# Optimization experiments

Hardware: AMD Instinct MI355X
Metric: run time of the kernel (lower is better)

The kernel has to match this reference:

```python
import jax, jax.numpy as jnp
import numpy as np

N_NODES = 100000
N_EDGES = 1600000
OBS_DIMS = 128
HID = 128
ACT_DIMS = 8
NUM_GRAPHS = 256
NEG_SLOPE = 0.2


def setup_inputs() -> dict:
    key = jax.random.key(0)
    ks = jax.random.split(key, 20)
    inp = {}
    inp["x"] = jax.random.normal(ks[0], (N_NODES, OBS_DIMS), dtype=jnp.float32)
    inp["edge_index"] = jax.random.randint(ks[1], (2, N_EDGES), 0, N_NODES, dtype=jnp.int64)
    inp["batch"] = jnp.sort(jax.random.randint(ks[2], (N_NODES,), 0, NUM_GRAPHS, dtype=jnp.int64))
    # GATConv layer params (heads=1): W [out,in], att_src/att_dst [out], bias [out]
    dims = [(HID, OBS_DIMS), (HID, HID), (HID, HID)]
    for i, (o, c) in enumerate(dims, start=1):
        k = 3 + 4 * (i - 1)
        inp[f"W{i}"] = jax.random.normal(ks[k], (o, c), dtype=jnp.float32) * (1.0 / np.sqrt(c))
        inp[f"as{i}"] = jax.random.normal(ks[k + 1], (o,), dtype=jnp.float32) * 0.1
        inp[f"ad{i}"] = jax.random.normal(ks[k + 2], (o,), dtype=jnp.float32) * 0.1
        inp[f"b{i}"] = jnp.zeros((o,), dtype=jnp.float32)
    inp["Wl"] = jax.random.normal(ks[15], (ACT_DIMS, HID), dtype=jnp.float32) * (1.0 / np.sqrt(HID))
    inp["bl"] = jnp.zeros((ACT_DIMS,), dtype=jnp.float32)
    return inp


def _gat_conv(x, src, dst, W, att_src, att_dst, bias):
    """PyG GATConv with heads=1, negative_slope=0.2 (self-loops already in src/dst)."""
    h = x @ W.T                                  # [N, out]
    a_s = h @ att_src                            # [N]
    a_d = h @ att_dst                            # [N]
    e = jax.nn.leaky_relu(a_s[src] + a_d[dst], NEG_SLOPE)   # [E] per-edge logits
    m = jax.ops.segment_max(e, dst, num_segments=N_NODES)   # segment softmax (stable)
    ex = jnp.exp(e - m[dst])
    denom = jax.ops.segment_sum(ex, dst, num_segments=N_NODES)
    alpha = ex / denom[dst]                      # [E]
    out = jax.ops.segment_sum(alpha[:, None] * h[src], dst, num_segments=N_NODES)
    return out + bias


def reference(x, edge_index, batch, W1, as1, ad1, b1, W2, as2, ad2, b2,
              W3, as3, ad3, b3, Wl, bl):
    # add self-loops (PyG GATConv default add_self_loops=True)
    loop = jnp.arange(N_NODES, dtype=edge_index.dtype)
    src = jnp.concatenate([edge_index[0], loop])
    dst = jnp.concatenate([edge_index[1], loop])

    h = jax.nn.relu(_gat_conv(x, src, dst, W1, as1, ad1, b1))
    h = jax.nn.relu(_gat_conv(h, src, dst, W2, as2, ad2, b2))
    h = jax.nn.relu(_gat_conv(h, src, dst, W3, as3, ad3, b3))
    h = jnp.tanh(h @ Wl.T + bl)                  # [N, act_dims]

    # global_mean_pool over graph ids
    sums = jax.ops.segment_sum(h, batch, num_segments=NUM_GRAPHS)
    cnts = jax.ops.segment_sum(jnp.ones((h.shape[0],), h.dtype), batch, num_segments=NUM_GRAPHS)
    return sums / jnp.clip(cnts, 1.0)[:, None]
```

## Files before the change

kernel.cpp:

```cpp
#include <hip/hip_runtime.h>

#define N_NODES 100000
#define N_EDGES 1600000
#define E_TOT   1700000
#define HID     128
#define NGRAPH  256
#define NBUCK   196
#define NBLK1   831
#define HSTRIDE 832

typedef unsigned short ushort_t;
typedef unsigned int uint_t;
typedef __attribute__((ext_vector_type(8))) short bf16x8;
typedef __attribute__((ext_vector_type(4))) float f32x4;

__device__ inline ushort_t f2bf(float f) {
  uint_t u = __float_as_uint(f);
  return (ushort_t)((u + 0x7FFFu + ((u >> 16) & 1u)) >> 16);
}

__global__ __launch_bounds__(256) void k_wcvt(const float* __restrict__ W0,
                                              const float* __restrict__ W1,
                                              const float* __restrict__ W2,
                                              const float* __restrict__ Wlh,
                                              ushort_t* __restrict__ Wb,
                                              ushort_t* __restrict__ Wlb) {
  int i = blockIdx.x * 256 + threadIdx.x;
  if (i < 49152) {
    const float* src = (i < 16384) ? W0 : (i < 32768 ? W1 : W2);
    Wb[i] = f2bf(src[i & 16383]);
  } else if (i < 51200) {
    int j = i - 49152;
    Wlb[j] = (j < 1024) ? f2bf(Wlh[j]) : (ushort_t)0;
  }
}

__global__ __launch_bounds__(256) void k_b1(const int* __restrict__ ei,
                                            int* __restrict__ hist) {
  __shared__ int h[NBUCK];
  const int t = threadIdx.x;
  for (int i = t; i < NBUCK; i += 256) h[i] = 0;
  __syncthreads();
  const int e0 = blockIdx.x * 2048;
#pragma unroll
  for (int u = 0; u < 8; ++u) {
    int e = e0 + u * 256 + t;
    if (e < E_TOT) {
      int dst = (e < N_EDGES) ? ei[N_EDGES + e] : (e - N_EDGES);
      atomicAdd(&h[dst >> 9], 1);
    }
  }
  __syncthreads();
  for (int i = t; i < NBUCK; i += 256) hist[i * HSTRIDE + blockIdx.x] = h[i];
}

__global__ __launch_bounds__(1024) void k_bscan1(int* __restrict__ hist,
                                                 int* __restrict__ btot) {
  __shared__ int sh[1024];
  const int b = blockIdx.x, t = threadIdx.x;
  int v = (t < NBLK1) ? hist[b * HSTRIDE + t] : 0;
  sh[t] = v;
  __syncthreads();
  for (int off = 1; off < 1024; off <<= 1) {
    int x = (t >= off) ? sh[t - off] : 0;
    __syncthreads();
    sh[t] += x;
    __syncthreads();
  }
  if (t < NBLK1) hist[b * HSTRIDE + t] = sh[t] - v;
  if (t == 1023) btot[b] = sh[1023];
}

__global__ void k_bscan2(const int* __restrict__ btot, int* __restrict__ bbase) {
  if (threadIdx.x == 0 && blockIdx.x == 0) {
    int run = 0;
    for (int i = 0; i < NBUCK; ++i) { bbase[i] = run; run += btot[i]; }
    bbase[NBUCK] = run;
  }
}

__global__ __launch_bounds__(256) void k_b2(const int* __restrict__ ei,
                                            const int* __restrict__ hist,
                                            const int* __restrict__ bbase,
                                            int2* __restrict__ buf) {
  __shared__ int h[NBUCK];
  __shared__ int base2[NBUCK];
  const int t = threadIdx.x;
  for (int i = t; i < NBUCK; i += 256) {
    h[i] = 0;
    base2[i] = bbase[i] + hist[i * HSTRIDE + blockIdx.x];
  }
  __syncthreads();
  const int e0 = blockIdx.x * 2048;
#pragma unroll
  for (int u = 0; u < 8; ++u) {
    int e = e0 + u * 256 + t;
    if (e < E_TOT) {
      int src, dst;
      if (e < N_EDGES) { src = ei[e]; dst = ei[N_EDGES + e]; }
      else             { src = e - N_EDGES; dst = src; }
      int bk = dst >> 9;
      int r = atomicAdd(&h[bk], 1);
      buf[base2[bk] + r] = int2{src, dst};
    }
  }
}

__global__ __launch_bounds__(512) void k_b3(const int2* __restrict__ buf,
                                            const int* __restrict__ bbase,
                                            int* __restrict__ indptr,
                                            int* __restrict__ csr_src) {
  __shared__ int cnt[512];
  __shared__ int cur[512];
  const int b = blockIdx.x, t = threadIdx.x;
  cnt[t] = 0;
  __syncthreads();
  const int es = bbase[b], ee = bbase[b + 1];
  for (int e = es + t; e < ee; e += 512) {
    int2 p = buf[e];
    atomicAdd(&cnt[p.y & 511], 1);
  }
  __syncthreads();
  int v = cnt[t];
  cur[t] = v;
  __syncthreads();
  for (int off = 1; off < 512; off <<= 1) {
    int x = (t >= off) ? cur[t - off] : 0;
    __syncthreads();
    cur[t] += x;
    __syncthreads();
  }
  int excl = cur[t] - v;
  int n = b * 512 + t;
  if (n < N_NODES) indptr[n] = es + excl;
  if (b == NBUCK - 1 && t == 0) indptr[N_NODES] = E_TOT;
  __syncthreads();
  cur[t] = es + excl;
  __syncthreads();
  for (int e = es + t; e < ee; e += 512) {
    int2 p = buf[e];
    int pos = atomicAdd(&cur[p.y & 511], 1);
    csr_src[pos] = p.x;
  }
}

template <bool IN_F32>
__global__ __launch_bounds__(256) void k_gemm(const void* __restrict__ Xin,
                                              const ushort_t* __restrict__ Wbl,
                                              const float* __restrict__ att_s,
                                              const float* __restrict__ att_d,
                                              ushort_t* __restrict__ Hb,
                                              float* __restrict__ As,
                                              float* __restrict__ Ad) {
  __shared__ ushort_t Wl[128 * 128];
  __shared__ ushort_t Xl[64 * 128];
  const int t = threadIdx.x;
  const int row0 = blockIdx.x * 64;

#pragma unroll
  for (int i = 0; i < 8; ++i) {
    int idx = (t + i * 256) << 3;
    int o = idx >> 7, c = idx & 127;
    uint4 wv = *(const uint4*)&Wbl[idx];
    *(uint4*)((char*)Wl + o * 256 + ((c * 2) ^ ((o & 7) << 4))) = wv;
  }
  if (IN_F32) {
    const float* X = (const float*)Xin;
#pragma unroll
    for (int i = 0; i < 8; ++i) {
      int idx = (t + i * 256) << 2;
      int r = idx >> 7, c = idx & 127;
      int row = row0 + r;
      float4 xv = (row < N_NODES) ? *(const float4*)&X[row * 128 + c]
                                  : float4{0.f, 0.f, 0.f, 0.f};
      ushort4 xb{f2bf(xv.x), f2bf(xv.y), f2bf(xv.z), f2bf(xv.w)};
      *(ushort4*)((char*)Xl + r * 256 + ((c * 2) ^ ((r & 7) << 4))) = xb;
    }
  } else {
    const ushort_t* X = (const ushort_t*)Xin;
#pragma unroll
    for (int i = 0; i < 4; ++i) {
      int idx = (t + i * 256) << 3;
      int r = idx >> 7, c = idx & 127;
      int row = row0 + r;
      uint4 xv = (row < N_NODES) ? *(const uint4*)&X[row * 128 + c]
                                 : uint4{0u, 0u, 0u, 0u};
      *(uint4*)((char*)Xl + r * 256 + ((c * 2) ^ ((r & 7) << 4))) = xv;
    }
  }
  __syncthreads();

  const int wv = t >> 6;
  const int lane = t & 63;
  const int lr = lane & 15;
  const int lg = lane >> 4;
  f32x4 acc[8] = {};

#pragma unroll
  for (int ks = 0; ks < 4; ++ks) {
    const int kbyte = ks * 64 + lg * 16;
    const int arow = wv * 16 + lr;
    bf16x8 afrag = *(const bf16x8*)((char*)Xl + arow * 256 +
                                    (kbyte ^ ((arow & 7) << 4)));
#pragma unroll
    for (int ot = 0; ot < 8; ++ot) {
      const int orow = ot * 16 + lr;
      bf16x8 bfrag = *(const bf16x8*)((char*)Wl + orow * 256 +
                                      (kbyte ^ ((orow & 7) << 4)));
      acc[ot] = __builtin_amdgcn_mfma_f32_16x16x32_bf16(afrag, bfrag, acc[ot],
                                                        0, 0, 0);
    }
  }

  float ps[4] = {0.f, 0.f, 0.f, 0.f}, pd[4] = {0.f, 0.f, 0.f, 0.f};
#pragma unroll
  for (int ot = 0; ot < 8; ++ot) {
    float sa = att_s[ot * 16 + lr], sd = att_d[ot * 16 + lr];
#pragma unroll
    for (int j = 0; j < 4; ++j) {
      ps[j] += acc[ot][j] * sa;
      pd[j] += acc[ot][j] * sd;
    }
  }
#pragma unroll
  for (int m = 1; m < 16; m <<= 1) {
#pragma unroll
    for (int j = 0; j < 4; ++j) {
      ps[j] += __shfl_xor(ps[j], m);
      pd[j] += __shfl_xor(pd[j], m);
    }
  }
  if (lr == 0) {
#pragma unroll
    for (int j = 0; j < 4; ++j) {
      int row = row0 + wv * 16 + lg * 4 + j;
      if (row < N_NODES) { As[row] = ps[j]; Ad[row] = pd[j]; }
    }
  }

  __syncthreads();
#pragma unroll
  for (int ot = 0; ot < 8; ++ot)
#pragma unroll
    for (int j = 0; j < 4; ++j) {
      int r = wv * 16 + lg * 4 + j;
      int cbyte = (ot * 16 + lr) * 2;
      *(ushort_t*)((char*)Xl + r * 256 + (cbyte ^ ((r & 7) << 4))) =
          f2bf(acc[ot][j]);
    }
  __syncthreads();
#pragma unroll
  for (int i = 0; i < 4; ++i) {
    int idx = t + i * 256;
    int r = idx >> 4, u = idx & 15;
    int row = row0 + r;
    if (row < N_NODES)
      *(uint4*)&Hb[row * 128 + u * 8] =
          *(const uint4*)((char*)Xl + r * 256 + ((u * 16) ^ ((r & 7) << 4)));
  }
}

__global__ __launch_bounds__(256) void k_agg(const ushort_t* __restrict__ Hb,
                                             const float* __restrict__ a_s,
                                             const float* __restrict__ a_d,
                                             const int* __restrict__ indptr,
                                             const int* __restrict__ csr_src,
                                             const float* __restrict__ bias,
                                             ushort_t* __restrict__ OUTb) {
  const int lane = threadIdx.x & 63;
  const int wid  = threadIdx.x >> 6;
  const int half = lane >> 5;
  const int l32  = lane & 31;
  const int n = blockIdx.x * 8 + wid * 2 + half;

  const int start = indptr[n];
  const int deg   = indptr[n + 1] - start;
  const float adn = a_d[n];

  int   s0 = csr_src[start + ((l32 < deg) ? l32 : 0)];
  float w0 = 0.f;
  if (l32 < deg) {
    float e = a_s[s0] + adn;
    e = (e > 0.f) ? e : 0.2f * e;
    w0 = __expf(e);
  }
  float wsum = w0;

  const int degA = __shfl(deg, 0);
  const int degB = __shfl(deg, 32);
  const int degM = max(degA, degB);

  const int q  = lane >> 4;
  const int qe = q & 1;
  const int srcbase = (q >> 1) << 5;
  const int ch = (lane & 15) << 3;
  float acc8[8] = {0.f, 0.f, 0.f, 0.f, 0.f, 0.f, 0.f, 0.f};

#define FMA8(W4, A)                                                         \
  {                                                                         \
    float a_ = (A);                                                         \
    acc8[0] += a_ * __uint_as_float((W4).x << 16);                          \
    acc8[1] += a_ * __uint_as_float((W4).x & 0xFFFF0000u);                  \
    acc8[2] += a_ * __uint_as_float((W4).y << 16);                          \
    acc8[3] += a_ * __uint_as_float((W4).y & 0xFFFF0000u);                  \
    acc8[4] += a_ * __uint_as_float((W4).z << 16);                          \
    acc8[5] += a_ * __uint_as_float((W4).z & 0xFFFF0000u);                  \
    acc8[6] += a_ * __uint_as_float((W4).w << 16);                          \
    acc8[7] += a_ * __uint_as_float((W4).w & 0xFFFF0000u);                  \
  }

  {
    const int npM = (min(degM, 32) + 1) >> 1;
    float av[8]; int sv[8];
#pragma unroll
    for (int u = 0; u < 8; ++u) {
      int sl = srcbase + ((u << 1) + qe);
      av[u] = __shfl(w0, sl);
      sv[u] = __shfl(s0, sl);
    }
    uint4 hvA[4], hvB[4];
#pragma unroll
    for (int u = 0; u < 4; ++u)
      if (u < npM) hvA[u] = *(const uint4*)&Hb[sv[u] * 128 + ch];
#pragma unroll
    for (int u = 0; u < 4; ++u)
      if (u + 4 < npM) hvB[u] = *(const uint4*)&Hb[sv[u + 4] * 128 + ch];
#pragma unroll
    for (int u = 0; u < 4; ++u)
      if (u < npM) FMA8(hvA[u], av[u]);
#pragma unroll
    for (int u = 0; u < 4; ++u)
      if (u + 4 < npM) FMA8(hvB[u], av[u + 4]);
    for (int u0 = 8; u0 < npM; ++u0) {
      int sl = srcbase + ((u0 << 1) + qe);
      float a = __shfl(w0, sl);
      int s = __shfl(s0, sl);
      uint4 hv = *(const uint4*)&Hb[s * 128 + ch];
      FMA8(hv, a);
    }
  }
  for (int base = 32; base < degM; base += 32) {
    int j = base + l32;
    int mys = csr_src[start + ((j < deg) ? j : 0)];
    float myw = 0.f;
    if (j < deg) {
      float e = a_s[mys] + adn;
      e = (e > 0.f) ? e : 0.2f * e;
      myw = __expf(e);
    }
    wsum += myw;
    const int npM = (min(degM - base, 32) + 1) >> 1;
    for (int u0 = 0; u0 < npM; ++u0) {
      int sl = srcbase + ((u0 << 1) + qe);
      float a = __shfl(myw, sl);
      int s = __shfl(mys, sl);
      uint4 hv = *(const uint4*)&Hb[s * 128 + ch];
      FMA8(hv, a);
    }
  }
#undef FMA8

#pragma unroll
  for (int m = 1; m < 32; m <<= 1) wsum += __shfl_xor(wsum, m);
  const float inv = 1.0f / wsum;

#pragma unroll
  for (int c = 0; c < 8; ++c)
    acc8[c] = (acc8[c] + __shfl_xor(acc8[c], 16)) * inv;

  if (qe == 0) {
    float4 b0 = *(const float4*)&bias[ch];
    float4 b1 = *(const float4*)&bias[ch + 4];
    ushort4 lo{f2bf(fmaxf(acc8[0] + b0.x, 0.f)),
               f2bf(fmaxf(acc8[1] + b0.y, 0.f)),
               f2bf(fmaxf(acc8[2] + b0.z, 0.f)),
               f2bf(fmaxf(acc8[3] + b0.w, 0.f))};
    ushort4 hi{f2bf(fmaxf(acc8[4] + b1.x, 0.f)),
               f2bf(fmaxf(acc8[5] + b1.y, 0.f)),
               f2bf(fmaxf(acc8[6] + b1.z, 0.f)),
               f2bf(fmaxf(acc8[7] + b1.w, 0.f))};
    *(ushort4*)&OUTb[n * 128 + ch] = lo;
    *(ushort4*)&OUTb[n * 128 + ch + 4] = hi;
  }
}

__global__ __launch_bounds__(256) void k_head(const ushort_t* __restrict__ Hb,
                                              const ushort_t* __restrict__ Wlb,
                                              const float* __restrict__ bl,
                                              float* __restrict__ h8) {
  __shared__ ushort_t Xl[64 * 128];
  __shared__ ushort_t Wls[16 * 128];
  const int t = threadIdx.x;
  const int row0 = blockIdx.x * 64;

  {
    int idx = t * 8;
    int o = idx >> 7, c = idx & 127;
    uint4 wv = *(const uint4*)&Wlb[idx];
    *(uint4*)((char*)Wls + o * 256 + ((c * 2) ^ ((o & 7) << 4))) = wv;
  }
#pragma unroll
  for (int i = 0; i < 4; ++i) {
    int idx = (t + i * 256) << 3;
    int r = idx >> 7, c = idx & 127;
    int row = row0 + r;
    uint4 xv = (row < N_NODES) ? *(const uint4*)&Hb[row * 128 + c]
                               : uint4{0u, 0u, 0u, 0u};
    *(uint4*)((char*)Xl + r * 256 + ((c * 2) ^ ((r & 7) << 4))) = xv;
  }
  __syncthreads();

  const int wv = t >> 6;
  const int lane = t & 63;
  const int lr = lane & 15;
  const int lg = lane >> 4;
  f32x4 acc = {};
#pragma unroll
  for (int ks = 0; ks < 4; ++ks) {
    const int kbyte = ks * 64 + lg * 16;
    const int arow = wv * 16 + lr;
    bf16x8 afrag = *(const bf16x8*)((char*)Xl + arow * 256 +
                                    (kbyte ^ ((arow & 7) << 4)));
    bf16x8 bfrag = *(const bf16x8*)((char*)Wls + lr * 256 +
                                    (kbyte ^ ((lr & 7) << 4)));
    acc = __builtin_amdgcn_mfma_f32_16x16x32_bf16(afrag, bfrag, acc, 0, 0, 0);
  }

  if (lr < 8) {
    float b = bl[lr];
#pragma unroll
    for (int j = 0; j < 4; ++j) {
      int row = row0 + wv * 16 + lg * 4 + j;
      if (row < N_NODES) h8[row * 8 + lr] = tanhf(acc[j] + b);
    }
  }
}

__global__ __launch_bounds__(256) void k_pool(const float* __restrict__ h8,
                                              const int* __restrict__ batch,
                                              float* __restrict__ out) {
  int g = blockIdx.x;
  __shared__ int bounds[2];
  if (threadIdx.x < 2) {
    int target = g + threadIdx.x;
    int lo = 0, hi = N_NODES;
    while (lo < hi) {
      int mid = (lo + hi) >> 1;
      if (batch[mid] < target) lo = mid + 1; else hi = mid;
    }
    bounds[threadIdx.x] = lo;
  }
  __syncthreads();
  int lo = bounds[0], hi = bounds[1];
  int ch = threadIdx.x & 7;
  float acc = 0.f;
  for (int n = lo + (threadIdx.x >> 3); n < hi; n += 32)
    acc += h8[n * 8 + ch];

  __shared__ float red[256];
  red[threadIdx.x] = acc;
  __syncthreads();
  for (int off = 128; off >= 8; off >>= 1) {
    if (threadIdx.x < off) red[threadIdx.x] += red[threadIdx.x + off];
    __syncthreads();
  }
  if (threadIdx.x < 8)
    out[g * 8 + threadIdx.x] = red[threadIdx.x] / fmaxf((float)(hi - lo), 1.0f);
}

extern "C" void kernel_launch(void* const* d_in, const int* in_sizes, int n_in,
                              void* d_out, int out_size, void* d_ws, size_t ws_size,
                              hipStream_t stream) {
  const float* x   = (const float*)d_in[0];
  const int*   ei  = (const int*)d_in[1];
  const int*   bat = (const int*)d_in[2];
  const float* Wm[3]  = {(const float*)d_in[3],  (const float*)d_in[7],  (const float*)d_in[11]};
  const float* asv[3] = {(const float*)d_in[4],  (const float*)d_in[8],  (const float*)d_in[12]};
  const float* adv[3] = {(const float*)d_in[5],  (const float*)d_in[9],  (const float*)d_in[13]};
  const float* bv[3]  = {(const float*)d_in[6],  (const float*)d_in[10], (const float*)d_in[14]};
  const float* Wl  = (const float*)d_in[15];
  const float* bl  = (const float*)d_in[16];
  float* out = (float*)d_out;

  char* w = (char*)d_ws;
  ushort_t* Hb   = (ushort_t*)(w + 0);
  ushort_t* hB2  = (ushort_t*)(w + 25600000);
  float* a_s     = (float*)(w + 51200000);
  float* a_d     = (float*)(w + 51600000);
  int*   indptr  = (int*)  (w + 52000000);
  int*   csr     = (int*)  (w + 52400128);
  int2*  buf1    = (int2*) (w + 59200128);
  int*   hist    = (int*)  (w + 72800128);
  int*   btot    = (int*)  (w + 73452416);
  int*   bbase   = (int*)  (w + 73453200);
  float* h8      = (float*)(w + 73454000);
  ushort_t* Wb   = (ushort_t*)(w + 76654000);
  ushort_t* Wlb  = (ushort_t*)(w + 76752304);

  const int gblk = (N_NODES + 63) / 64;
  const int ablk = N_NODES / 8;

  k_wcvt<<<200, 256, 0, stream>>>(Wm[0], Wm[1], Wm[2], Wl, Wb, Wlb);

  k_b1    <<<NBLK1, 256, 0, stream>>>(ei, hist);
  k_bscan1<<<NBUCK, 1024, 0, stream>>>(hist, btot);
  k_bscan2<<<1, 64, 0, stream>>>(btot, bbase);
  k_b2    <<<NBLK1, 256, 0, stream>>>(ei, hist, bbase, buf1);
  k_b3    <<<NBUCK, 512, 0, stream>>>(buf1, bbase, indptr, csr);

  k_gemm<true><<<gblk, 256, 0, stream>>>(x, Wb, asv[0], adv[0], Hb, a_s, a_d);
  k_agg<<<ablk, 256, 0, stream>>>(Hb, a_s, a_d, indptr, csr, bv[0], hB2);
  for (int l = 1; l < 3; ++l) {
    k_gemm<false><<<gblk, 256, 0, stream>>>(hB2, Wb + l * 16384, asv[l], adv[l],
                                            Hb, a_s, a_d);
    k_agg<<<ablk, 256, 0, stream>>>(Hb, a_s, a_d, indptr, csr, bv[l], hB2);
  }

  k_head<<<gblk, 256, 0, stream>>>(hB2, Wlb, bl, h8);
  k_pool<<<NGRAPH, 256, 0, stream>>>(h8, bat, out);
}
```

Baseline: 314.5 us.

## Pack CSR bucket entries into one int, enlarge GEMM row tile, restructure agg loop

```diff
diff --git a/kernel.cpp b/kernel.cpp
--- a/kernel.cpp
+++ b/kernel.cpp
@@ -82,7 +82,7 @@
 __global__ __launch_bounds__(256) void k_b2(const int* __restrict__ ei,
                                             const int* __restrict__ hist,
                                             const int* __restrict__ bbase,
-                                            int2* __restrict__ buf) {
+                                            int* __restrict__ buf) {
   __shared__ int h[NBUCK];
   __shared__ int base2[NBUCK];
   const int t = threadIdx.x;
@@ -101,12 +101,12 @@
       else             { src = e - N_EDGES; dst = src; }
       int bk = dst >> 9;
       int r = atomicAdd(&h[bk], 1);
-      buf[base2[bk] + r] = int2{src, dst};
-    }
-  }
-}
-
-__global__ __launch_bounds__(512) void k_b3(const int2* __restrict__ buf,
+      buf[base2[bk] + r] = (src << 9) | (dst & 511);
+    }
+  }
+}
+
+__global__ __launch_bounds__(512) void k_b3(const int* __restrict__ buf,
                                             const int* __restrict__ bbase,
                                             int* __restrict__ indptr,
                                             int* __restrict__ csr_src) {
@@ -116,10 +116,8 @@
   cnt[t] = 0;
   __syncthreads();
   const int es = bbase[b], ee = bbase[b + 1];
-  for (int e = es + t; e < ee; e += 512) {
-    int2 p = buf[e];
-    atomicAdd(&cnt[p.y & 511], 1);
-  }
+  for (int e = es + t; e < ee; e += 512)
+    atomicAdd(&cnt[buf[e] & 511], 1);
   __syncthreads();
   int v = cnt[t];
   cur[t] = v;
@@ -138,9 +136,9 @@
   cur[t] = es + excl;
   __syncthreads();
   for (int e = es + t; e < ee; e += 512) {
-    int2 p = buf[e];
-    int pos = atomicAdd(&cur[p.y & 511], 1);
-    csr_src[pos] = p.x;
+    int p = buf[e];
+    int pos = atomicAdd(&cur[p & 511], 1);
+    csr_src[pos] = p >> 9;
   }
 }
 
@@ -153,9 +151,9 @@
                                               float* __restrict__ As,
                                               float* __restrict__ Ad) {
   __shared__ ushort_t Wl[128 * 128];
-  __shared__ ushort_t Xl[64 * 128];
+  __shared__ ushort_t Xl[128 * 128];
   const int t = threadIdx.x;
-  const int row0 = blockIdx.x * 64;
+  const int row0 = blockIdx.x * 128;
 
 #pragma unroll
   for (int i = 0; i < 8; ++i) {
@@ -167,7 +165,7 @@
   if (IN_F32) {
     const float* X = (const float*)Xin;
 #pragma unroll
-    for (int i = 0; i < 8; ++i) {
+    for (int i = 0; i < 16; ++i) {
       int idx = (t + i * 256) << 2;
       int r = idx >> 7, c = idx & 127;
       int row = row0 + r;
@@ -179,7 +177,7 @@
   } else {
     const ushort_t* X = (const ushort_t*)Xin;
 #pragma unroll
-    for (int i = 0; i < 4; ++i) {
+    for (int i = 0; i < 8; ++i) {
       int idx = (t + i * 256) << 3;
       int r = idx >> 7, c = idx & 127;
       int row = row0 + r;
@@ -194,63 +192,77 @@
   const int lane = t & 63;
   const int lr = lane & 15;
   const int lg = lane >> 4;
-  f32x4 acc[8] = {};
+  f32x4 acc[2][8] = {};
 
 #pragma unroll
   for (int ks = 0; ks < 4; ++ks) {
     const int kbyte = ks * 64 + lg * 16;
-    const int arow = wv * 16 + lr;
-    bf16x8 afrag = *(const bf16x8*)((char*)Xl + arow * 256 +
-                                    (kbyte ^ ((arow & 7) << 4)));
+    bf16x8 afrag[2];
+#pragma unroll
+    for (int rt = 0; rt < 2; ++rt) {
+      const int arow = wv * 32 + rt * 16 + lr;
+      afrag[rt] = *(const bf16x8*)((char*)Xl + arow * 256 +
+                                   (kbyte ^ ((arow & 7) << 4)));
+    }
 #pragma unroll
     for (int ot = 0; ot < 8; ++ot) {
       const int orow = ot * 16 + lr;
       bf16x8 bfrag = *(const bf16x8*)((char*)Wl + orow * 256 +
                                       (kbyte ^ ((orow & 7) << 4)));
-      acc[ot] = __builtin_amdgcn_mfma_f32_16x16x32_bf16(afrag, bfrag, acc[ot],
-                                                        0, 0, 0);
-    }
-  }
-
-  float ps[4] = {0.f, 0.f, 0.f, 0.f}, pd[4] = {0.f, 0.f, 0.f, 0.f};
+#pragma unroll
+      for (int rt = 0; rt < 2; ++rt)
+        acc[rt][ot] = __builtin_amdgcn_mfma_f32_16x16x32_bf16(
+            afrag[rt], bfrag, acc[rt][ot], 0, 0, 0);
+    }
+  }
+
+  float ps[2][4] = {{0.f}}, pd[2][4] = {{0.f}};
 #pragma unroll
   for (int ot = 0; ot < 8; ++ot) {
     float sa = att_s[ot * 16 + lr], sd = att_d[ot * 16 + lr];
 #pragma unroll
-    for (int j = 0; j < 4; ++j) {
-      ps[j] += acc[ot][j] * sa;
-      pd[j] += acc[ot][j] * sd;
-    }
+    for (int rt = 0; rt < 2; ++rt)
+#pragma unroll
+      for (int j = 0; j < 4; ++j) {
+        ps[rt][j] += acc[rt][ot][j] * sa;
+        pd[rt][j] += acc[rt][ot][j] * sd;
+      }
   }
 #pragma unroll
   for (int m = 1; m < 16; m <<= 1) {
 #pragma unroll
-    for (int j = 0; j < 4; ++j) {
-      ps[j] += __shfl_xor(ps[j], m);
-      pd[j] += __shfl_xor(pd[j], m);
-    }
+    for (int rt = 0; rt < 2; ++rt)
+#pragma unroll
+      for (int j = 0; j < 4; ++j) {
+        ps[rt][j] += __shfl_xor(ps[rt][j], m);
+        pd[rt][j] += __shfl_xor(pd[rt][j], m);
+      }
   }
   if (lr == 0) {
 #pragma unroll
-    for (int j = 0; j < 4; ++j) {
-      int row = row0 + wv * 16 + lg * 4 + j;
-      if (row < N_NODES) { As[row] = ps[j]; Ad[row] = pd[j]; }
-    }
-  }
-
-  __syncthreads();
-#pragma unroll
-  for (int ot = 0; ot < 8; ++ot)
-#pragma unroll
-    for (int j = 0; j < 4; ++j) {
-      int r = wv * 16 + lg * 4 + j;
-      int cbyte = (ot * 16 + lr) * 2;
-      *(ushort_t*)((char*)Xl + r * 256 + (cbyte ^ ((r & 7) << 4))) =
-          f2bf(acc[ot][j]);
-    }
-  __syncthreads();
-#pragma unroll
-  for (int i = 0; i < 4; ++i) {
+    for (int rt = 0; rt < 2; ++rt)
+#pragma unroll
+      for (int j = 0; j < 4; ++j) {
+        int row = row0 + wv * 32 + rt * 16 + lg * 4 + j;
+        if (row < N_NODES) { As[row] = ps[rt][j]; Ad[row] = pd[rt][j]; }
+      }
+  }
+
+  __syncthreads();
+#pragma unroll
+  for (int rt = 0; rt < 2; ++rt)
+#pragma unroll
+    for (int ot = 0; ot < 8; ++ot)
+#pragma unroll
+      for (int j = 0; j < 4; ++j) {
+        int r = wv * 32 + rt * 16 + lg * 4 + j;
+        int cbyte = (ot * 16 + lr) * 2;
+        *(ushort_t*)((char*)Xl + r * 256 + (cbyte ^ ((r & 7) << 4))) =
+            f2bf(acc[rt][ot][j]);
+      }
+  __syncthreads();
+#pragma unroll
+  for (int i = 0; i < 8; ++i) {
     int idx = t + i * 256;
     int r = idx >> 4, u = idx & 15;
     int row = row0 + r;
@@ -309,48 +321,40 @@
     acc8[7] += a_ * __uint_as_float((W4).w & 0xFFFF0000u);                  \
   }
 
-  {
-    const int npM = (min(degM, 32) + 1) >> 1;
-    float av[8]; int sv[8];
-#pragma unroll
-    for (int u = 0; u < 8; ++u) {
-      int sl = srcbase + ((u << 1) + qe);
-      av[u] = __shfl(w0, sl);
-      sv[u] = __shfl(s0, sl);
-    }
-    uint4 hvA[4], hvB[4];
-#pragma unroll
-    for (int u = 0; u < 4; ++u)
-      if (u < npM) hvA[u] = *(const uint4*)&Hb[sv[u] * 128 + ch];
-#pragma unroll
-    for (int u = 0; u < 4; ++u)
-      if (u + 4 < npM) hvB[u] = *(const uint4*)&Hb[sv[u + 4] * 128 + ch];
-#pragma unroll
-    for (int u = 0; u < 4; ++u)
-      if (u < npM) FMA8(hvA[u], av[u]);
-#pragma unroll
-    for (int u = 0; u < 4; ++u)
-      if (u + 4 < npM) FMA8(hvB[u], av[u + 4]);
-    for (int u0 = 8; u0 < npM; ++u0) {
-      int sl = srcbase + ((u0 << 1) + qe);
-      float a = __shfl(w0, sl);
-      int s = __shfl(s0, sl);
-      uint4 hv = *(const uint4*)&Hb[s * 128 + ch];
-      FMA8(hv, a);
-    }
-  }
-  for (int base = 32; base < degM; base += 32) {
-    int j = base + l32;
-    int mys = csr_src[start + ((j < deg) ? j : 0)];
-    float myw = 0.f;
-    if (j < deg) {
-      float e = a_s[mys] + adn;
-      e = (e > 0.f) ? e : 0.2f * e;
-      myw = __expf(e);
-    }
-    wsum += myw;
+  for (int base = 0; base < degM; base += 32) {
+    float myw;
+    int mys;
+    if (base == 0) {
+      myw = w0;
+      mys = s0;
+    } else {
+      int j = base + l32;
+      mys = csr_src[start + ((j < deg) ? j : 0)];
+      myw = 0.f;
+      if (j < deg) {
+        float e = a_s[mys] + adn;
+        e = (e > 0.f) ? e : 0.2f * e;
+        myw = __expf(e);
+      }
+      wsum += myw;
+    }
     const int npM = (min(degM - base, 32) + 1) >> 1;
-    for (int u0 = 0; u0 < npM; ++u0) {
+    int u0 = 0;
+    for (; u0 + 4 <= npM; u0 += 4) {
+      float av[4]; int sv[4]; uint4 hv[4];
+#pragma unroll
+      for (int u = 0; u < 4; ++u) {
+        int sl = srcbase + (((u0 + u) << 1) + qe);
+        av[u] = __shfl(myw, sl);
+        sv[u] = __shfl(mys, sl);
+      }
+#pragma unroll
+      for (int u = 0; u < 4; ++u)
+        hv[u] = *(const uint4*)&Hb[sv[u] * 128 + ch];
+#pragma unroll
+      for (int u = 0; u < 4; ++u) FMA8(hv[u], av[u]);
+    }
+    for (; u0 < npM; ++u0) {
       int sl = srcbase + ((u0 << 1) + qe);
       float a = __shfl(myw, sl);
       int s = __shfl(mys, sl);
@@ -489,7 +493,7 @@
   float* a_d     = (float*)(w + 51600000);
   int*   indptr  = (int*)  (w + 52000000);
   int*   csr     = (int*)  (w + 52400128);
-  int2*  buf1    = (int2*) (w + 59200128);
+  int*   buf1    = (int*)  (w + 59200128);
   int*   hist    = (int*)  (w + 72800128);
   int*   btot    = (int*)  (w + 73452416);
   int*   bbase   = (int*)  (w + 73453200);
@@ -497,7 +501,8 @@
   ushort_t* Wb   = (ushort_t*)(w + 76654000);
   ushort_t* Wlb  = (ushort_t*)(w + 76752304);
 
-  const int gblk = (N_NODES + 63) / 64;
+  const int gblk = (N_NODES + 127) / 128;
+  const int hblk = (N_NODES + 63) / 64;
   const int ablk = N_NODES / 8;
 
   k_wcvt<<<200, 256, 0, stream>>>(Wm[0], Wm[1], Wm[2], Wl, Wb, Wlb);
@@ -516,6 +521,6 @@
     k_agg<<<ablk, 256, 0, stream>>>(Hb, a_s, a_d, indptr, csr, bv[l], hB2);
   }
 
-  k_head<<<gblk, 256, 0, stream>>>(hB2, Wlb, bl, h8);
+  k_head<<<hblk, 256, 0, stream>>>(hB2, Wlb, bl, h8);
   k_pool<<<NGRAPH, 256, 0, stream>>>(h8, bat, out);
 }
```

After: 316.6 us. About the same (+0.7%).
